# Optimization experiments

Hardware: AMD Instinct MI355X
Metric: run time of the kernel (lower is better)

Reference implementation:

```python
import jax, jax.numpy as jnp
import numpy as np

N, E, H, D_IN, D_OUT, DEPTH, G = 100000, 1600000, 128, 128, 10, 3, 256


def setup_inputs() -> dict:
    key = jax.random.key(0)
    ks = jax.random.split(key, 16)
    s = lambda k, shape: jax.random.normal(k, shape, dtype=jnp.float32) * 0.05
    inp = {
        "x": jax.random.normal(ks[0], (N, D_IN), dtype=jnp.float32),
        "edge_index": jax.random.randint(ks[1], (2, E), 0, N, dtype=jnp.int32),
        "control_edge_index": jax.random.randint(ks[2], (2, 1024), 0, N, dtype=jnp.int32),
        "batch": jnp.sort(jax.random.randint(ks[3], (N,), 0, G, dtype=jnp.int32)),
        # encoder MLP: input_dim -> hidden -> hidden
        "enc_w1": s(ks[4], (D_IN, H)), "enc_b1": jnp.zeros((H,), jnp.float32),
        "enc_w2": s(ks[5], (H, H)),    "enc_b2": jnp.zeros((H,), jnp.float32),
        # conv_depth GCN layers, hidden -> hidden
        "conv_w": s(ks[6], (DEPTH, H, H)), "conv_b": jnp.zeros((DEPTH, H), jnp.float32),
        # decoder MLP: hidden -> hidden -> output_dim
        "dec_w1": s(ks[7], (H, H)),     "dec_b1": jnp.zeros((H,), jnp.float32),
        "dec_w2": s(ks[8], (H, D_OUT)), "dec_b2": jnp.zeros((D_OUT,), jnp.float32),
    }
    return inp


def _gcn_forward(x, enc_w1, enc_b1, enc_w2, enc_b2, conv_w, conv_b,
                 dec_w1, dec_b1, dec_w2, dec_b2, edge_index, batch):
    # encoder MLP (Linear-ReLU-Dropout(eval)-Linear)
    h = jax.nn.relu(x @ enc_w1 + enc_b1) @ enc_w2 + enc_b2

    # GCN normalization with self-loops: D^{-1/2} (A + I) D^{-1/2}
    loops = jnp.arange(N, dtype=edge_index.dtype)
    src = jnp.concatenate([edge_index[0], loops])  # [E + N]
    dst = jnp.concatenate([edge_index[1], loops])
    deg = jax.ops.segment_sum(jnp.ones_like(src, dtype=h.dtype), dst, num_segments=N)
    inv_sqrt = jax.lax.rsqrt(deg)  # deg >= 1 thanks to self-loops
    coef = (inv_sqrt[src] * inv_sqrt[dst])[:, None]  # [E+N, 1]

    for l in range(DEPTH):
        hw = h @ conv_w[l] + conv_b[l]                      # [N, H]
        h = jax.ops.segment_sum(hw[src] * coef, dst, num_segments=N)
        if l < DEPTH - 1:  # linear=False -> nonlinearity between convs
            h = jax.nn.relu(h)

    # global_add_pool over graph ids
    pooled = jax.ops.segment_sum(h, batch, num_segments=G)   # [G, H]

    # decoder MLP
    return jax.nn.relu(pooled @ dec_w1 + dec_b1) @ dec_w2 + dec_b2  # [G, D_OUT]


def reference(x, edge_index, control_edge_index, batch, enc_w1, enc_b1, enc_w2,
              enc_b2, conv_w, conv_b, dec_w1, dec_b1, dec_w2, dec_b2):
    # control_edge_index corresponds to the (disabled) control mechanism; unused
    return _gcn_forward(x, enc_w1, enc_b1, enc_w2, enc_b2, conv_w, conv_b,
                        dec_w1, dec_b1, dec_w2, dec_b2, edge_index, batch)
```

## Files before the change

kernel.cpp:

```cpp
#include <hip/hip_runtime.h>
#include <hip/hip_bf16.h>
#include <cstdint>
#include <cstddef>

#define NN 100000
#define NE 1600000
#define HH 128
#define NG 256

#define NB 196
#define BSH 9
#define BMSK 511
#define CHUNK 16384
#define NBLK 98

typedef __bf16 bf16x8 __attribute__((ext_vector_type(8)));
typedef float floatx4 __attribute__((ext_vector_type(4)));

__device__ __forceinline__ uint32_t f2b(float f) {
  union { float f; uint32_t u; } v; v.f = f;
  uint32_t u = v.u;
  return (u + 0x7FFFu + ((u >> 16) & 1u)) >> 16;
}
__device__ __forceinline__ float b2f(uint32_t h) {
  union { uint32_t u; float f; } v; v.u = h << 16;
  return v.f;
}
__device__ __forceinline__ void addrow(float* a, uint4 v) {
  a[0] += b2f(v.x & 0xFFFFu); a[1] += b2f(v.x >> 16);
  a[2] += b2f(v.y & 0xFFFFu); a[3] += b2f(v.y >> 16);
  a[4] += b2f(v.z & 0xFFFFu); a[5] += b2f(v.z >> 16);
  a[6] += b2f(v.w & 0xFFFFu); a[7] += b2f(v.w >> 16);
}


__global__ __launch_bounds__(256) void k_cntA(const int* __restrict__ src,
                                              int* __restrict__ blkcnt) {
  __shared__ int h[NB];
  int t = threadIdx.x;
  if (t < NB) h[t] = 0;
  __syncthreads();
  int base = blockIdx.x * CHUNK, end = min(base + CHUNK, NE);
  for (int i = base + t; i < end; i += 256) atomicAdd(&h[src[i] >> BSH], 1);
  __syncthreads();
  if (t < NB) blkcnt[blockIdx.x * NB + t] = h[t];
}

__global__ __launch_bounds__(256) void k_cntB(const uint2* __restrict__ pairs,
                                              int* __restrict__ blkcnt) {
  __shared__ int h[NB];
  int t = threadIdx.x;
  if (t < NB) h[t] = 0;
  __syncthreads();
  int base = blockIdx.x * CHUNK, end = min(base + CHUNK, NE);
  for (int i = base + t; i < end; i += 256) atomicAdd(&h[pairs[i].y >> BSH], 1);
  __syncthreads();
  if (t < NB) blkcnt[blockIdx.x * NB + t] = h[t];
}

__global__ __launch_bounds__(64) void k_colscan(const int* __restrict__ blkcnt,
                                                int* __restrict__ poff,
                                                int* __restrict__ colsum) {
  int b = blockIdx.x, t = threadIdx.x;
  int carry = 0;
  for (int base = 0; base < NBLK; base += 64) {
    int r = base + t;
    int x = (r < NBLK) ? blkcnt[r * NB + b] : 0;
    int v = x;
    for (int d = 1; d < 64; d <<= 1) { int u = __shfl_up(v, d); if (t >= d) v += u; }
    if (r < NBLK) poff[r * NB + b] = carry + v - x;
    carry += __shfl(v, 63);
  }
  if (t == 0) colsum[b] = carry;
}

__global__ void k_gscan(const int* __restrict__ colsum, int* __restrict__ gbase,
                        int* __restrict__ off, int set_off) {
  __shared__ int s[256];
  int t = threadIdx.x;
  int x = (t < NB) ? colsum[t] : 0;
  s[t] = x; __syncthreads();
  for (int d = 1; d < 256; d <<= 1) {
    int v = (t >= d) ? s[t - d] : 0;
    __syncthreads();
    s[t] += v;
    __syncthreads();
  }
  if (t < NB) gbase[t] = s[t] - x;
  if (t == 0) { gbase[NB] = NE; if (set_off) off[NN] = NE; }
}

__global__ __launch_bounds__(256) void k_placeA(const int* __restrict__ src,
                                                const int* __restrict__ dst,
                                                const int* __restrict__ poff,
                                                const int* __restrict__ gbase,
                                                uint2* __restrict__ pairs) {
  __shared__ int cur[NB];
  int t = threadIdx.x;
  if (t < NB) cur[t] = poff[blockIdx.x * NB + t] + gbase[t];
  __syncthreads();
  int base = blockIdx.x * CHUNK, end = min(base + CHUNK, NE);
  for (int i = base + t; i < end; i += 256) {
    int s = src[i], d = dst[i];
    int p = atomicAdd(&cur[s >> BSH], 1);
    pairs[p] = make_uint2((unsigned)s, (unsigned)d);
  }
}

__global__ __launch_bounds__(256) void k_placeB(const uint2* __restrict__ pairs,
                                                const int* __restrict__ poff,
                                                const int* __restrict__ gbase,
                                                uint32_t* __restrict__ outb) {
  __shared__ int cur[NB];
  int t = threadIdx.x;
  if (t < NB) cur[t] = poff[blockIdx.x * NB + t] + gbase[t];
  __syncthreads();
  int base = blockIdx.x * CHUNK, end = min(base + CHUNK, NE);
  for (int i = base + t; i < end; i += 256) {
    uint2 v = pairs[i];
    int p = atomicAdd(&cur[v.y >> BSH], 1);
    outb[p] = v.x | ((v.y & (unsigned)BMSK) << 17);
  }
}

__global__ __launch_bounds__(256) void k_bucket_sort(
    const uint32_t* __restrict__ pairbuf, const int* __restrict__ gbase,
    int* __restrict__ off, float* __restrict__ inv, int* __restrict__ csrs)
{
  __shared__ int cnt[512];
  __shared__ int loff[512];
  __shared__ int psum[256];
  int b = blockIdx.x;
  int tid = threadIdx.x;
  cnt[tid] = 0; cnt[tid + 256] = 0;
  __syncthreads();
  int s0 = gbase[b], s1 = gbase[b + 1];
  for (int i = s0 + tid; i < s1; i += 256)
    atomicAdd(&cnt[pairbuf[i] >> 17], 1);
  __syncthreads();
  int a0 = cnt[2 * tid], a1 = cnt[2 * tid + 1];
  int s = a0 + a1;
  psum[tid] = s;
  __syncthreads();
  for (int d = 1; d < 256; d <<= 1) {
    int v = (tid >= d) ? psum[tid - d] : 0;
    __syncthreads();
    psum[tid] += v;
    __syncthreads();
  }
  int excl = psum[tid] - s;
  loff[2 * tid] = excl;
  loff[2 * tid + 1] = excl + a0;
  __syncthreads();
#pragma unroll
  for (int k = 0; k < 2; ++k) {
    int i = tid + k * 256;
    int node = b * 512 + i;
    if (node < NN) {
      off[node] = s0 + loff[i];
      inv[node] = rsqrtf((float)cnt[i] + 1.0f);
    }
  }
  __syncthreads();
  cnt[tid] = loff[tid]; cnt[tid + 256] = loff[tid + 256];
  __syncthreads();
  for (int i = s0 + tid; i < s1; i += 256) {
    uint32_t v = pairbuf[i];
    int p = atomicAdd(&cnt[v >> 17], 1);
    csrs[s0 + p] = (int)(v & 0x1FFFFu);
  }
}

__global__ __launch_bounds__(256) void k_nodeprep(const int* __restrict__ off,
                                                  const int* __restrict__ batch,
                                                  int* __restrict__ dhist,
                                                  int* __restrict__ gstart) {
  __shared__ int h[64];
  int t = threadIdx.x;
  if (t < 64) h[t] = 0;
  __syncthreads();
  int i = blockIdx.x * 256 + t;
  if (i < NN) {
    int d = off[i + 1] - off[i]; if (d > 63) d = 63;
    atomicAdd(&h[d], 1);
    int b = batch[i];
    if (i == 0) {
      for (int g = 0; g <= b; ++g) gstart[g] = 0;
    } else {
      int a = batch[i - 1];
      for (int g = a + 1; g <= b; ++g) gstart[g] = i;
    }
    if (i == NN - 1) {
      for (int g = b + 1; g <= NG; ++g) gstart[g] = NN;
    }
  }
  __syncthreads();
  if (t < 64 && h[t]) atomicAdd(&dhist[t], h[t]);
}

__global__ void k_dscan(const int* __restrict__ dhist, int* __restrict__ dcur) {
  int t = threadIdx.x;
  int x = dhist[63 - t];
  int v = x;
  for (int d = 1; d < 64; d <<= 1) { int u = __shfl_up(v, d); if (t >= d) v += u; }
  dcur[63 - t] = v - x;
}

__global__ __launch_bounds__(256) void k_dplace(const int* __restrict__ off,
                                                int* __restrict__ dcur,
                                                int* __restrict__ order) {
  __shared__ int h[64], base[64];
  int t = threadIdx.x;
  if (t < 64) h[t] = 0;
  __syncthreads();
  int i = blockIdx.x * 256 + t;
  int d = 0, ld = 0;
  if (i < NN) { d = off[i + 1] - off[i]; if (d > 63) d = 63; ld = atomicAdd(&h[d], 1); }
  __syncthreads();
  if (t < 64) base[t] = h[t] ? atomicAdd(&dcur[t], h[t]) : 0;
  __syncthreads();
  if (i < NN) order[base[d] + ld] = i;
}

__global__ __launch_bounds__(256) void k_gemm(
    const uint16_t* __restrict__ A16, const float* __restrict__ A32,
    const float* __restrict__ W, const float* __restrict__ bias,
    const float* __restrict__ scale,
    uint16_t* __restrict__ Out, int M, int do_relu)
{
  __shared__ uint16_t Wt[128][136];
  const int tid = threadIdx.x;

  for (int it = 0; it < 16; ++it) {
    int idx = tid + it * 256;
    int n = idx & 127;
    int k0 = (idx >> 7) * 4;
    uint2 wv;
    wv.x = f2b(W[(k0 + 0) * 128 + n]) | (f2b(W[(k0 + 1) * 128 + n]) << 16);
    wv.y = f2b(W[(k0 + 2) * 128 + n]) | (f2b(W[(k0 + 3) * 128 + n]) << 16);
    *(uint2*)&Wt[n][k0] = wv;
  }
  __syncthreads();

  const int lane = tid & 63;
  const int wave = tid >> 6;
  const int lrow = lane & 15;
  const int lk = (lane >> 4) * 8;
  const int row0 = blockIdx.x * 128 + wave * 32;

  floatx4 acc[2][8];
#pragma unroll
  for (int t = 0; t < 2; ++t)
#pragma unroll
    for (int n = 0; n < 8; ++n)
      acc[t][n] = (floatx4){0.f, 0.f, 0.f, 0.f};

#pragma unroll
  for (int ks = 0; ks < 4; ++ks) {
    bf16x8 a[2];
#pragma unroll
    for (int t = 0; t < 2; ++t) {
      int r = row0 + t * 16 + lrow;
      uint4 tmp = {0u, 0u, 0u, 0u};
      if (r < M) {
        if (A32) {
          float4 f0 = *(const float4*)(A32 + (size_t)r * HH + ks * 32 + lk);
          float4 f1 = *(const float4*)(A32 + (size_t)r * HH + ks * 32 + lk + 4);
          tmp.x = f2b(f0.x) | (f2b(f0.y) << 16);
          tmp.y = f2b(f0.z) | (f2b(f0.w) << 16);
          tmp.z = f2b(f1.x) | (f2b(f1.y) << 16);
          tmp.w = f2b(f1.z) | (f2b(f1.w) << 16);
        } else {
          tmp = *(const uint4*)(A16 + (size_t)r * HH + ks * 32 + lk);
        }
      }
      a[t] = __builtin_bit_cast(bf16x8, tmp);
    }
#pragma unroll
    for (int n = 0; n < 8; ++n) {
      bf16x8 b = __builtin_bit_cast(bf16x8, *(const uint4*)&Wt[n * 16 + lrow][ks * 32 + lk]);
      acc[0][n] = __builtin_amdgcn_mfma_f32_16x16x32_bf16(a[0], b, acc[0][n], 0, 0, 0);
      acc[1][n] = __builtin_amdgcn_mfma_f32_16x16x32_bf16(a[1], b, acc[1][n], 0, 0, 0);
    }
  }

  float bc[8];
#pragma unroll
  for (int n = 0; n < 8; ++n) bc[n] = bias[n * 16 + lrow];

  const int rbase = (lane >> 4) * 4;
#pragma unroll
  for (int t = 0; t < 2; ++t) {
#pragma unroll
    for (int r = 0; r < 4; ++r) {
      int row = row0 + t * 16 + rbase + r;
      if (row < M) {
        float sc = scale ? scale[row] : 1.0f;
#pragma unroll
        for (int n = 0; n < 8; ++n) {
          float v = acc[t][n][r] + bc[n];
          if (do_relu) v = fmaxf(v, 0.f);
          v *= sc;
          Out[(size_t)row * HH + n * 16 + lrow] = (uint16_t)f2b(v);
        }
      }
    }
  }
}

__global__ __launch_bounds__(256) void k_agg(
    const uint16_t* __restrict__ hw2, const int* __restrict__ off,
    const int* __restrict__ csrs, const float* __restrict__ inv,
    const int* __restrict__ order,
    uint16_t* __restrict__ hout, int do_relu)
{
  int slot = blockIdx.x * 16 + (threadIdx.x >> 4);
  if (slot >= NN) return;
  int node = order[slot];
  int c = (threadIdx.x & 15) * 8;

  uint4 sv = *(const uint4*)(hw2 + (size_t)node * HH + c);
  float a[8] = {0.f, 0.f, 0.f, 0.f, 0.f, 0.f, 0.f, 0.f};
  addrow(a, sv);

  int e0 = off[node], e1 = off[node + 1];
  int e = e0;
  for (; e + 4 <= e1; e += 4) {
    int s0 = csrs[e + 0], s1 = csrs[e + 1], s2 = csrs[e + 2], s3 = csrs[e + 3];
    uint4 v0 = *(const uint4*)(hw2 + (size_t)s0 * HH + c);
    uint4 v1 = *(const uint4*)(hw2 + (size_t)s1 * HH + c);
    uint4 v2 = *(const uint4*)(hw2 + (size_t)s2 * HH + c);
    uint4 v3 = *(const uint4*)(hw2 + (size_t)s3 * HH + c);
    addrow(a, v0); addrow(a, v1); addrow(a, v2); addrow(a, v3);
  }
  for (; e < e1; ++e) {
    int s = csrs[e];
    uint4 v = *(const uint4*)(hw2 + (size_t)s * HH + c);
    addrow(a, v);
  }
  float invd = inv[node];
#pragma unroll
  for (int j = 0; j < 8; ++j) {
    a[j] *= invd;
    if (do_relu) a[j] = fmaxf(a[j], 0.f);
  }
  uint4 o;
  o.x = f2b(a[0]) | (f2b(a[1]) << 16);
  o.y = f2b(a[2]) | (f2b(a[3]) << 16);
  o.z = f2b(a[4]) | (f2b(a[5]) << 16);
  o.w = f2b(a[6]) | (f2b(a[7]) << 16);
  *(uint4*)(hout + (size_t)node * HH + c) = o;
}

__global__ __launch_bounds__(256) void k_pool(const uint16_t* __restrict__ h,
                                              const int* __restrict__ gstart,
                                              float* __restrict__ pooled) {
  __shared__ float red[16][132];
  int g = blockIdx.x;
  int tid = threadIdx.x;
  int slot = tid >> 4;
  int c = (tid & 15) * 8;

  int r0 = gstart[g], r1 = gstart[g + 1];
  float a[8] = {0.f, 0.f, 0.f, 0.f, 0.f, 0.f, 0.f, 0.f};
  for (int r = r0 + slot; r < r1; r += 16) {
    uint4 v = *(const uint4*)(h + (size_t)r * HH + c);
    a[0] += b2f(v.x & 0xFFFFu); a[1] += b2f(v.x >> 16);
    a[2] += b2f(v.y & 0xFFFFu); a[3] += b2f(v.y >> 16);
    a[4] += b2f(v.z & 0xFFFFu); a[5] += b2f(v.z >> 16);
    a[6] += b2f(v.w & 0xFFFFu); a[7] += b2f(v.w >> 16);
  }
  *(float4*)&red[slot][c]     = make_float4(a[0], a[1], a[2], a[3]);
  *(float4*)&red[slot][c + 4] = make_float4(a[4], a[5], a[6], a[7]);
  __syncthreads();
  if (tid < 128) {
    float s = 0.f;
#pragma unroll
    for (int k = 0; k < 16; ++k) s += red[k][tid];
    pooled[g * HH + tid] = s;
  }
}

__global__ void k_dec(const float* __restrict__ pooled,
                      const float* __restrict__ w1, const float* __restrict__ b1,
                      const float* __restrict__ w2, const float* __restrict__ b2,
                      float* __restrict__ out) {
  __shared__ float p[128], t[128];
  int g = blockIdx.x, j = threadIdx.x;
  p[j] = pooled[g * HH + j];
  __syncthreads();
  float a = b1[j];
  for (int k = 0; k < 128; ++k) a += p[k] * w1[k * 128 + j];
  t[j] = fmaxf(a, 0.f);
  __syncthreads();
  if (j < 10) {
    float o = b2[j];
    for (int k = 0; k < 128; ++k) o += t[k] * w2[k * 10 + j];
    out[g * 10 + j] = o;
  }
}

extern "C" void kernel_launch(void* const* d_in, const int* in_sizes, int n_in,
                              void* d_out, int out_size, void* d_ws, size_t ws_size,
                              hipStream_t stream) {
  const float* x       = (const float*)d_in[0];
  const int*   eidx    = (const int*)d_in[1];
  const int*   src     = eidx;
  const int*   dst     = eidx + NE;
  const int*   batch   = (const int*)d_in[3];
  const float* enc_w1  = (const float*)d_in[4];
  const float* enc_b1  = (const float*)d_in[5];
  const float* enc_w2  = (const float*)d_in[6];
  const float* enc_b2  = (const float*)d_in[7];
  const float* conv_w  = (const float*)d_in[8];
  const float* conv_b  = (const float*)d_in[9];
  const float* dec_w1  = (const float*)d_in[10];
  const float* dec_b1  = (const float*)d_in[11];
  const float* dec_w2  = (const float*)d_in[12];
  const float* dec_b2  = (const float*)d_in[13];
  float* out = (float*)d_out;

  char* ws = (char*)d_ws;
  size_t o = 0;
  auto alloc = [&](size_t bytes) -> char* {
    char* p = ws + o;
    o += (bytes + 255) & ~(size_t)255;
    return p;
  };
  int*      off     = (int*)alloc((size_t)(NN + 1) * 4);
  int*      csrs    = (int*)alloc((size_t)NE * 4);
  float*    inv     = (float*)alloc((size_t)NN * 4);
  float*    pooled  = (float*)alloc((size_t)NG * HH * 4);
  int*      blkcntA = (int*)alloc((size_t)NBLK * NB * 4);
  int*      poffA   = (int*)alloc((size_t)NBLK * NB * 4);
  int*      blkcntB = (int*)alloc((size_t)NBLK * NB * 4);
  int*      poffB   = (int*)alloc((size_t)NBLK * NB * 4);
  int*      colsumA = (int*)alloc((size_t)NB * 4);
  int*      colsumB = (int*)alloc((size_t)NB * 4);
  int*      gbaseA  = (int*)alloc((size_t)(NB + 1) * 4);
  int*      gbaseB  = (int*)alloc((size_t)(NB + 1) * 4);
  int*      dhist   = (int*)alloc(64 * 4);
  int*      dcur    = (int*)alloc(64 * 4);
  int*      order   = (int*)alloc((size_t)NN * 4);
  int*      gstart  = (int*)alloc((size_t)(NG + 1) * 4);
  uint16_t* buf0    = (uint16_t*)alloc((size_t)NN * HH * 2);
  uint16_t* buf1    = (uint16_t*)alloc((size_t)NN * HH * 2);
  uint2*    pairsA  = (uint2*)buf1;
  uint32_t* pairB   = (uint32_t*)((char*)buf1 + (size_t)NE * 8);

  hipMemsetAsync(dhist, 0, 64 * 4, stream);

  k_cntA<<<dim3(NBLK), dim3(256), 0, stream>>>(src, blkcntA);
  k_colscan<<<dim3(NB), dim3(64), 0, stream>>>(blkcntA, poffA, colsumA);
  k_gscan<<<dim3(1), dim3(256), 0, stream>>>(colsumA, gbaseA, off, 0);
  k_placeA<<<dim3(NBLK), dim3(256), 0, stream>>>(src, dst, poffA, gbaseA, pairsA);
  k_cntB<<<dim3(NBLK), dim3(256), 0, stream>>>(pairsA, blkcntB);
  k_colscan<<<dim3(NB), dim3(64), 0, stream>>>(blkcntB, poffB, colsumB);
  k_gscan<<<dim3(1), dim3(256), 0, stream>>>(colsumB, gbaseB, off, 1);
  k_placeB<<<dim3(NBLK), dim3(256), 0, stream>>>(pairsA, poffB, gbaseB, pairB);
  k_bucket_sort<<<dim3(NB), dim3(256), 0, stream>>>(pairB, gbaseB, off, inv, csrs);

  const int NBK = (NN + 255) / 256;
  k_nodeprep<<<dim3(NBK), dim3(256), 0, stream>>>(off, batch, dhist, gstart);
  k_dscan<<<dim3(1), dim3(64), 0, stream>>>(dhist, dcur);
  k_dplace<<<dim3(NBK), dim3(256), 0, stream>>>(off, dcur, order);

  const int GB = (NN + 127) / 128;
  k_gemm<<<dim3(GB), dim3(256), 0, stream>>>(nullptr, x, enc_w1, enc_b1, nullptr, buf1, NN, 1);
  k_gemm<<<dim3(GB), dim3(256), 0, stream>>>(buf1, nullptr, enc_w2, enc_b2, nullptr, buf0, NN, 0);

  const int AB = (NN + 15) / 16;
  k_gemm<<<dim3(GB), dim3(256), 0, stream>>>(buf0, nullptr, conv_w + 0 * 16384, conv_b + 0,   inv, buf1, NN, 0);
  k_agg <<<dim3(AB), dim3(256), 0, stream>>>(buf1, off, csrs, inv, order, buf0, 1);
  k_gemm<<<dim3(GB), dim3(256), 0, stream>>>(buf0, nullptr, conv_w + 1 * 16384, conv_b + 128, inv, buf1, NN, 0);
  k_agg <<<dim3(AB), dim3(256), 0, stream>>>(buf1, off, csrs, inv, order, buf0, 1);
  k_gemm<<<dim3(GB), dim3(256), 0, stream>>>(buf0, nullptr, conv_w + 2 * 16384, conv_b + 256, inv, buf1, NN, 0);
  k_agg <<<dim3(AB), dim3(256), 0, stream>>>(buf1, off, csrs, inv, order, buf0, 0);

  k_pool<<<dim3(NG), dim3(256), 0, stream>>>(buf0, gstart, pooled);
  k_dec<<<dim3(NG), dim3(128), 0, stream>>>(pooled, dec_w1, dec_b1, dec_w2, dec_b2, out);
}
```

Baseline: 523.9 us.

## Fuse CSR build into one cooperative kernel and merge pool with decoder

The dozen graph-preprocessing launches (counting, column scans, placement, bucket sort, node prep, degree-sorted ordering) are merged into one cooperative kernel of 196 blocks that uses grid-wide syncs between phases. Edge chunks are resized so each of the 196 blocks takes one slice, and the degree histogram becomes per-block partials summed by block 0, which removes the memset and the global atomics. Pooling and the decoder MLP are fused into one kernel, dropping the intermediate pooled buffer. The aim is to cut launch overhead and inter-kernel gaps. The cost is grid-sync latency and fewer active blocks in the phases that used to launch 391 blocks.

Result: slower. 722.6 us (+37.9%).

```diff
diff --git a/kernel.cpp b/kernel.cpp
--- a/kernel.cpp
+++ b/kernel.cpp
@@ -1,7 +1,10 @@
 #include <hip/hip_runtime.h>
 #include <hip/hip_bf16.h>
+#include <hip/hip_cooperative_groups.h>
 #include <cstdint>
 #include <cstddef>
+
+namespace cg = cooperative_groups;
 
 #define NN 100000
 #define NE 1600000
@@ -11,8 +14,7 @@
 #define NB 196
 #define BSH 9
 #define BMSK 511
-#define CHUNK 16384
-#define NBLK 98
+#define ECH 8164
 
 typedef __bf16 bf16x8 __attribute__((ext_vector_type(8)));
 typedef float floatx4 __attribute__((ext_vector_type(4)));
@@ -33,193 +35,192 @@
   a[6] += b2f(v.w & 0xFFFFu); a[7] += b2f(v.w >> 16);
 }
 
-
-__global__ __launch_bounds__(256) void k_cntA(const int* __restrict__ src,
-                                              int* __restrict__ blkcnt) {
-  __shared__ int h[NB];
-  int t = threadIdx.x;
-  if (t < NB) h[t] = 0;
-  __syncthreads();
-  int base = blockIdx.x * CHUNK, end = min(base + CHUNK, NE);
-  for (int i = base + t; i < end; i += 256) atomicAdd(&h[src[i] >> BSH], 1);
-  __syncthreads();
-  if (t < NB) blkcnt[blockIdx.x * NB + t] = h[t];
-}
-
-__global__ __launch_bounds__(256) void k_cntB(const uint2* __restrict__ pairs,
-                                              int* __restrict__ blkcnt) {
-  __shared__ int h[NB];
-  int t = threadIdx.x;
-  if (t < NB) h[t] = 0;
-  __syncthreads();
-  int base = blockIdx.x * CHUNK, end = min(base + CHUNK, NE);
-  for (int i = base + t; i < end; i += 256) atomicAdd(&h[pairs[i].y >> BSH], 1);
-  __syncthreads();
-  if (t < NB) blkcnt[blockIdx.x * NB + t] = h[t];
-}
-
-__global__ __launch_bounds__(64) void k_colscan(const int* __restrict__ blkcnt,
-                                                int* __restrict__ poff,
-                                                int* __restrict__ colsum) {
-  int b = blockIdx.x, t = threadIdx.x;
-  int carry = 0;
-  for (int base = 0; base < NBLK; base += 64) {
-    int r = base + t;
-    int x = (r < NBLK) ? blkcnt[r * NB + b] : 0;
-    int v = x;
+struct BuildArgs {
+  const int* src; const int* dst; const int* batch;
+  int* blkcntA; int* poffA; int* colsumA; int* gbaseA;
+  uint2* pairsA;
+  int* blkcntB; int* poffB; int* colsumB; int* gbaseB;
+  uint32_t* pairB;
+  int* off; float* inv; int* csrs;
+  int* dhist2; int* dcur; int* order; int* gstart;
+};
+
+__global__ __launch_bounds__(256) void k_build(BuildArgs A) {
+  cg::grid_group grid = cg::this_grid();
+  __shared__ int sm[1536];
+  const int b = blockIdx.x, t = threadIdx.x;
+
+  {
+    int* h = sm;
+    if (t < NB) h[t] = 0;
+    __syncthreads();
+    int e0 = b * ECH, e1 = min(e0 + ECH, NE);
+    for (int i = e0 + t; i < e1; i += 256) atomicAdd(&h[A.src[i] >> BSH], 1);
+    __syncthreads();
+    if (t < NB) A.blkcntA[b * NB + t] = h[t];
+  }
+  grid.sync();
+  {
+    int* s = sm;
+    int x = (t < NB) ? A.blkcntA[t * NB + b] : 0;
+    s[t] = x; __syncthreads();
+    for (int d = 1; d < 256; d <<= 1) {
+      int v = (t >= d) ? s[t - d] : 0; __syncthreads(); s[t] += v; __syncthreads();
+    }
+    if (t < NB) A.poffA[t * NB + b] = s[t] - x;
+    if (t == 255) A.colsumA[b] = s[255];
+  }
+  grid.sync();
+  if (b == 0) {
+    int* s = sm;
+    int x = (t < NB) ? A.colsumA[t] : 0;
+    s[t] = x; __syncthreads();
+    for (int d = 1; d < 256; d <<= 1) {
+      int v = (t >= d) ? s[t - d] : 0; __syncthreads(); s[t] += v; __syncthreads();
+    }
+    if (t < NB) A.gbaseA[t] = s[t] - x;
+    if (t == 0) A.gbaseA[NB] = NE;
+  }
+  grid.sync();
+  {
+    int* cur = sm;
+    if (t < NB) cur[t] = A.poffA[b * NB + t] + A.gbaseA[t];
+    __syncthreads();
+    int e0 = b * ECH, e1 = min(e0 + ECH, NE);
+    for (int i = e0 + t; i < e1; i += 256) {
+      int s_ = A.src[i], d_ = A.dst[i];
+      int p = atomicAdd(&cur[s_ >> BSH], 1);
+      A.pairsA[p] = make_uint2((unsigned)s_, (unsigned)d_);
+    }
+  }
+  grid.sync();
+  {
+    int* h = sm;
+    if (t < NB) h[t] = 0;
+    __syncthreads();
+    int e0 = b * ECH, e1 = min(e0 + ECH, NE);
+    for (int i = e0 + t; i < e1; i += 256) atomicAdd(&h[A.pairsA[i].y >> BSH], 1);
+    __syncthreads();
+    if (t < NB) A.blkcntB[b * NB + t] = h[t];
+  }
+  grid.sync();
+  {
+    int* s = sm;
+    int x = (t < NB) ? A.blkcntB[t * NB + b] : 0;
+    s[t] = x; __syncthreads();
+    for (int d = 1; d < 256; d <<= 1) {
+      int v = (t >= d) ? s[t - d] : 0; __syncthreads(); s[t] += v; __syncthreads();
+    }
+    if (t < NB) A.poffB[t * NB + b] = s[t] - x;
+    if (t == 255) A.colsumB[b] = s[255];
+  }
+  grid.sync();
+  if (b == 0) {
+    int* s = sm;
+    int x = (t < NB) ? A.colsumB[t] : 0;
+    s[t] = x; __syncthreads();
+    for (int d = 1; d < 256; d <<= 1) {
+      int v = (t >= d) ? s[t - d] : 0; __syncthreads(); s[t] += v; __syncthreads();
+    }
+    if (t < NB) A.gbaseB[t] = s[t] - x;
+    if (t == 0) { A.gbaseB[NB] = NE; A.off[NN] = NE; }
+  }
+  grid.sync();
+  {
+    int* cur = sm;
+    if (t < NB) cur[t] = A.poffB[b * NB + t] + A.gbaseB[t];
+    __syncthreads();
+    int e0 = b * ECH, e1 = min(e0 + ECH, NE);
+    for (int i = e0 + t; i < e1; i += 256) {
+      uint2 v = A.pairsA[i];
+      int p = atomicAdd(&cur[v.y >> BSH], 1);
+      A.pairB[p] = v.x | ((v.y & (unsigned)BMSK) << 17);
+    }
+  }
+  grid.sync();
+  {
+    int* cnt = sm; int* loff = sm + 512; int* psum = sm + 1024;
+    cnt[t] = 0; cnt[t + 256] = 0;
+    __syncthreads();
+    int s0 = A.gbaseB[b], s1 = A.gbaseB[b + 1];
+    for (int i = s0 + t; i < s1; i += 256) atomicAdd(&cnt[A.pairB[i] >> 17], 1);
+    __syncthreads();
+    int a0 = cnt[2 * t], a1 = cnt[2 * t + 1];
+    int s = a0 + a1;
+    psum[t] = s; __syncthreads();
+    for (int d = 1; d < 256; d <<= 1) {
+      int v = (t >= d) ? psum[t - d] : 0; __syncthreads(); psum[t] += v; __syncthreads();
+    }
+    int excl = psum[t] - s;
+    loff[2 * t] = excl;
+    loff[2 * t + 1] = excl + a0;
+    __syncthreads();
+    int* h64 = psum;
+    if (t < 64) h64[t] = 0;
+    __syncthreads();
+#pragma unroll
+    for (int k = 0; k < 2; ++k) {
+      int i = t + k * 256;
+      int node = b * 512 + i;
+      if (node < NN) {
+        A.off[node] = s0 + loff[i];
+        A.inv[node] = rsqrtf((float)cnt[i] + 1.0f);
+        int d = cnt[i]; if (d > 63) d = 63;
+        atomicAdd(&h64[d], 1);
+      }
+    }
+    __syncthreads();
+    if (t < 64) A.dhist2[b * 64 + t] = h64[t];
+    int n0 = b * 512, n1 = min(n0 + 512, NN);
+    for (int i = n0 + t; i < n1; i += 256) {
+      int bb = A.batch[i];
+      if (i == 0) { for (int g = 0; g <= bb; ++g) A.gstart[g] = 0; }
+      else { int aa = A.batch[i - 1]; for (int g = aa + 1; g <= bb; ++g) A.gstart[g] = i; }
+      if (i == NN - 1) { for (int g = bb + 1; g <= NG; ++g) A.gstart[g] = NN; }
+    }
+    __syncthreads();
+    cnt[t] = loff[t]; cnt[t + 256] = loff[t + 256];
+    __syncthreads();
+    for (int i = s0 + t; i < s1; i += 256) {
+      uint32_t v = A.pairB[i];
+      int p = atomicAdd(&cnt[v >> 17], 1);
+      A.csrs[s0 + p] = (int)(v & 0x1FFFFu);
+    }
+  }
+  grid.sync();
+  if (b == 0 && t < 64) {
+    int sum = 0;
+    for (int r = 0; r < NB; ++r) sum += A.dhist2[r * 64 + (63 - t)];
+    int v = sum;
     for (int d = 1; d < 64; d <<= 1) { int u = __shfl_up(v, d); if (t >= d) v += u; }
-    if (r < NBLK) poff[r * NB + b] = carry + v - x;
-    carry += __shfl(v, 63);
-  }
-  if (t == 0) colsum[b] = carry;
-}
-
-__global__ void k_gscan(const int* __restrict__ colsum, int* __restrict__ gbase,
-                        int* __restrict__ off, int set_off) {
-  __shared__ int s[256];
-  int t = threadIdx.x;
-  int x = (t < NB) ? colsum[t] : 0;
-  s[t] = x; __syncthreads();
-  for (int d = 1; d < 256; d <<= 1) {
-    int v = (t >= d) ? s[t - d] : 0;
-    __syncthreads();
-    s[t] += v;
-    __syncthreads();
-  }
-  if (t < NB) gbase[t] = s[t] - x;
-  if (t == 0) { gbase[NB] = NE; if (set_off) off[NN] = NE; }
-}
-
-__global__ __launch_bounds__(256) void k_placeA(const int* __restrict__ src,
-                                                const int* __restrict__ dst,
-                                                const int* __restrict__ poff,
-                                                const int* __restrict__ gbase,
-                                                uint2* __restrict__ pairs) {
-  __shared__ int cur[NB];
-  int t = threadIdx.x;
-  if (t < NB) cur[t] = poff[blockIdx.x * NB + t] + gbase[t];
-  __syncthreads();
-  int base = blockIdx.x * CHUNK, end = min(base + CHUNK, NE);
-  for (int i = base + t; i < end; i += 256) {
-    int s = src[i], d = dst[i];
-    int p = atomicAdd(&cur[s >> BSH], 1);
-    pairs[p] = make_uint2((unsigned)s, (unsigned)d);
-  }
-}
-
-__global__ __launch_bounds__(256) void k_placeB(const uint2* __restrict__ pairs,
-                                                const int* __restrict__ poff,
-                                                const int* __restrict__ gbase,
-                                                uint32_t* __restrict__ outb) {
-  __shared__ int cur[NB];
-  int t = threadIdx.x;
-  if (t < NB) cur[t] = poff[blockIdx.x * NB + t] + gbase[t];
-  __syncthreads();
-  int base = blockIdx.x * CHUNK, end = min(base + CHUNK, NE);
-  for (int i = base + t; i < end; i += 256) {
-    uint2 v = pairs[i];
-    int p = atomicAdd(&cur[v.y >> BSH], 1);
-    outb[p] = v.x | ((v.y & (unsigned)BMSK) << 17);
-  }
-}
-
-__global__ __launch_bounds__(256) void k_bucket_sort(
-    const uint32_t* __restrict__ pairbuf, const int* __restrict__ gbase,
-    int* __restrict__ off, float* __restrict__ inv, int* __restrict__ csrs)
-{
-  __shared__ int cnt[512];
-  __shared__ int loff[512];
-  __shared__ int psum[256];
-  int b = blockIdx.x;
-  int tid = threadIdx.x;
-  cnt[tid] = 0; cnt[tid + 256] = 0;
-  __syncthreads();
-  int s0 = gbase[b], s1 = gbase[b + 1];
-  for (int i = s0 + tid; i < s1; i += 256)
-    atomicAdd(&cnt[pairbuf[i] >> 17], 1);
-  __syncthreads();
-  int a0 = cnt[2 * tid], a1 = cnt[2 * tid + 1];
-  int s = a0 + a1;
-  psum[tid] = s;
-  __syncthreads();
-  for (int d = 1; d < 256; d <<= 1) {
-    int v = (tid >= d) ? psum[tid - d] : 0;
-    __syncthreads();
-    psum[tid] += v;
-    __syncthreads();
-  }
-  int excl = psum[tid] - s;
-  loff[2 * tid] = excl;
-  loff[2 * tid + 1] = excl + a0;
-  __syncthreads();
-#pragma unroll
-  for (int k = 0; k < 2; ++k) {
-    int i = tid + k * 256;
-    int node = b * 512 + i;
-    if (node < NN) {
-      off[node] = s0 + loff[i];
-      inv[node] = rsqrtf((float)cnt[i] + 1.0f);
-    }
-  }
-  __syncthreads();
-  cnt[tid] = loff[tid]; cnt[tid + 256] = loff[tid + 256];
-  __syncthreads();
-  for (int i = s0 + tid; i < s1; i += 256) {
-    uint32_t v = pairbuf[i];
-    int p = atomicAdd(&cnt[v >> 17], 1);
-    csrs[s0 + p] = (int)(v & 0x1FFFFu);
-  }
-}
-
-__global__ __launch_bounds__(256) void k_nodeprep(const int* __restrict__ off,
-                                                  const int* __restrict__ batch,
-                                                  int* __restrict__ dhist,
-                                                  int* __restrict__ gstart) {
-  __shared__ int h[64];
-  int t = threadIdx.x;
-  if (t < 64) h[t] = 0;
-  __syncthreads();
-  int i = blockIdx.x * 256 + t;
-  if (i < NN) {
-    int d = off[i + 1] - off[i]; if (d > 63) d = 63;
-    atomicAdd(&h[d], 1);
-    int b = batch[i];
-    if (i == 0) {
-      for (int g = 0; g <= b; ++g) gstart[g] = 0;
-    } else {
-      int a = batch[i - 1];
-      for (int g = a + 1; g <= b; ++g) gstart[g] = i;
-    }
-    if (i == NN - 1) {
-      for (int g = b + 1; g <= NG; ++g) gstart[g] = NN;
-    }
-  }
-  __syncthreads();
-  if (t < 64 && h[t]) atomicAdd(&dhist[t], h[t]);
-}
-
-__global__ void k_dscan(const int* __restrict__ dhist, int* __restrict__ dcur) {
-  int t = threadIdx.x;
-  int x = dhist[63 - t];
-  int v = x;
-  for (int d = 1; d < 64; d <<= 1) { int u = __shfl_up(v, d); if (t >= d) v += u; }
-  dcur[63 - t] = v - x;
-}
-
-__global__ __launch_bounds__(256) void k_dplace(const int* __restrict__ off,
-                                                int* __restrict__ dcur,
-                                                int* __restrict__ order) {
-  __shared__ int h[64], base[64];
-  int t = threadIdx.x;
-  if (t < 64) h[t] = 0;
-  __syncthreads();
-  int i = blockIdx.x * 256 + t;
-  int d = 0, ld = 0;
-  if (i < NN) { d = off[i + 1] - off[i]; if (d > 63) d = 63; ld = atomicAdd(&h[d], 1); }
-  __syncthreads();
-  if (t < 64) base[t] = h[t] ? atomicAdd(&dcur[t], h[t]) : 0;
-  __syncthreads();
-  if (i < NN) order[base[d] + ld] = i;
+    A.dcur[63 - t] = v - sum;
+  }
+  grid.sync();
+  {
+    int* h = sm; int* base = sm + 64;
+    if (t < 64) h[t] = 0;
+    __syncthreads();
+    int dd[2], ld[2];
+    int n0 = b * 512;
+#pragma unroll
+    for (int k = 0; k < 2; ++k) {
+      int i = n0 + t + k * 256;
+      dd[k] = -1; ld[k] = 0;
+      if (i < NN) {
+        int d = A.off[i + 1] - A.off[i]; if (d > 63) d = 63;
+        dd[k] = d;
+        ld[k] = atomicAdd(&h[d], 1);
+      }
+    }
+    __syncthreads();
+    if (t < 64) base[t] = h[t] ? atomicAdd(&A.dcur[t], h[t]) : 0;
+    __syncthreads();
+#pragma unroll
+    for (int k = 0; k < 2; ++k) {
+      int i = n0 + t + k * 256;
+      if (i < NN) A.order[base[dd[k]] + ld[k]] = i;
+    }
+  }
 }
 
 __global__ __launch_bounds__(256) void k_gemm(
@@ -352,10 +353,14 @@
   *(uint4*)(hout + (size_t)node * HH + c) = o;
 }
 
-__global__ __launch_bounds__(256) void k_pool(const uint16_t* __restrict__ h,
-                                              const int* __restrict__ gstart,
-                                              float* __restrict__ pooled) {
+__global__ __launch_bounds__(256) void k_pooldec(
+    const uint16_t* __restrict__ h, const int* __restrict__ gstart,
+    const float* __restrict__ w1, const float* __restrict__ b1,
+    const float* __restrict__ w2, const float* __restrict__ b2,
+    float* __restrict__ out)
+{
   __shared__ float red[16][132];
+  __shared__ float p[128], tmpv[128];
   int g = blockIdx.x;
   int tid = threadIdx.x;
   int slot = tid >> 4;
@@ -377,26 +382,19 @@
     float s = 0.f;
 #pragma unroll
     for (int k = 0; k < 16; ++k) s += red[k][tid];
-    pooled[g * HH + tid] = s;
-  }
-}
-
-__global__ void k_dec(const float* __restrict__ pooled,
-                      const float* __restrict__ w1, const float* __restrict__ b1,
-                      const float* __restrict__ w2, const float* __restrict__ b2,
-                      float* __restrict__ out) {
-  __shared__ float p[128], t[128];
-  int g = blockIdx.x, j = threadIdx.x;
-  p[j] = pooled[g * HH + j];
+    p[tid] = s;
+  }
   __syncthreads();
-  float a = b1[j];
-  for (int k = 0; k < 128; ++k) a += p[k] * w1[k * 128 + j];
-  t[j] = fmaxf(a, 0.f);
+  if (tid < 128) {
+    float acc1 = b1[tid];
+    for (int k = 0; k < 128; ++k) acc1 += p[k] * w1[k * 128 + tid];
+    tmpv[tid] = fmaxf(acc1, 0.f);
+  }
   __syncthreads();
-  if (j < 10) {
-    float o = b2[j];
-    for (int k = 0; k < 128; ++k) o += t[k] * w2[k * 10 + j];
-    out[g * 10 + j] = o;
+  if (tid < 10) {
+    float o = b2[tid];
+    for (int k = 0; k < 128; ++k) o += tmpv[k] * w2[k * 10 + tid];
+    out[g * 10 + tid] = o;
   }
 }
 
@@ -430,16 +428,15 @@
   int*      off     = (int*)alloc((size_t)(NN + 1) * 4);
   int*      csrs    = (int*)alloc((size_t)NE * 4);
   float*    inv     = (float*)alloc((size_t)NN * 4);
-  float*    pooled  = (float*)alloc((size_t)NG * HH * 4);
-  int*      blkcntA = (int*)alloc((size_t)NBLK * NB * 4);
-  int*      poffA   = (int*)alloc((size_t)NBLK * NB * 4);
-  int*      blkcntB = (int*)alloc((size_t)NBLK * NB * 4);
-  int*      poffB   = (int*)alloc((size_t)NBLK * NB * 4);
+  int*      blkcntA = (int*)alloc((size_t)NB * NB * 4);
+  int*      poffA   = (int*)alloc((size_t)NB * NB * 4);
+  int*      blkcntB = (int*)alloc((size_t)NB * NB * 4);
+  int*      poffB   = (int*)alloc((size_t)NB * NB * 4);
   int*      colsumA = (int*)alloc((size_t)NB * 4);
   int*      colsumB = (int*)alloc((size_t)NB * 4);
   int*      gbaseA  = (int*)alloc((size_t)(NB + 1) * 4);
   int*      gbaseB  = (int*)alloc((size_t)(NB + 1) * 4);
-  int*      dhist   = (int*)alloc(64 * 4);
+  int*      dhist2  = (int*)alloc((size_t)NB * 64 * 4);
   int*      dcur    = (int*)alloc(64 * 4);
   int*      order   = (int*)alloc((size_t)NN * 4);
   int*      gstart  = (int*)alloc((size_t)(NG + 1) * 4);
@@ -448,22 +445,16 @@
   uint2*    pairsA  = (uint2*)buf1;
   uint32_t* pairB   = (uint32_t*)((char*)buf1 + (size_t)NE * 8);
 
-  hipMemsetAsync(dhist, 0, 64 * 4, stream);
-
-  k_cntA<<<dim3(NBLK), dim3(256), 0, stream>>>(src, blkcntA);
-  k_colscan<<<dim3(NB), dim3(64), 0, stream>>>(blkcntA, poffA, colsumA);
-  k_gscan<<<dim3(1), dim3(256), 0, stream>>>(colsumA, gbaseA, off, 0);
-  k_placeA<<<dim3(NBLK), dim3(256), 0, stream>>>(src, dst, poffA, gbaseA, pairsA);
-  k_cntB<<<dim3(NBLK), dim3(256), 0, stream>>>(pairsA, blkcntB);
-  k_colscan<<<dim3(NB), dim3(64), 0, stream>>>(blkcntB, poffB, colsumB);
-  k_gscan<<<dim3(1), dim3(256), 0, stream>>>(colsumB, gbaseB, off, 1);
-  k_placeB<<<dim3(NBLK), dim3(256), 0, stream>>>(pairsA, poffB, gbaseB, pairB);
-  k_bucket_sort<<<dim3(NB), dim3(256), 0, stream>>>(pairB, gbaseB, off, inv, csrs);
-
-  const int NBK = (NN + 255) / 256;
-  k_nodeprep<<<dim3(NBK), dim3(256), 0, stream>>>(off, batch, dhist, gstart);
-  k_dscan<<<dim3(1), dim3(64), 0, stream>>>(dhist, dcur);
-  k_dplace<<<dim3(NBK), dim3(256), 0, stream>>>(off, dcur, order);
+  BuildArgs ba;
+  ba.src = src; ba.dst = dst; ba.batch = batch;
+  ba.blkcntA = blkcntA; ba.poffA = poffA; ba.colsumA = colsumA; ba.gbaseA = gbaseA;
+  ba.pairsA = pairsA;
+  ba.blkcntB = blkcntB; ba.poffB = poffB; ba.colsumB = colsumB; ba.gbaseB = gbaseB;
+  ba.pairB = pairB;
+  ba.off = off; ba.inv = inv; ba.csrs = csrs;
+  ba.dhist2 = dhist2; ba.dcur = dcur; ba.order = order; ba.gstart = gstart;
+  void* bargs[] = { &ba };
+  hipLaunchCooperativeKernel((void*)k_build, dim3(NB), dim3(256), bargs, 0, stream);
 
   const int GB = (NN + 127) / 128;
   k_gemm<<<dim3(GB), dim3(256), 0, stream>>>(nullptr, x, enc_w1, enc_b1, nullptr, buf1, NN, 1);
@@ -477,6 +468,5 @@
   k_gemm<<<dim3(GB), dim3(256), 0, stream>>>(buf0, nullptr, conv_w + 2 * 16384, conv_b + 256, inv, buf1, NN, 0);
   k_agg <<<dim3(AB), dim3(256), 0, stream>>>(buf1, off, csrs, inv, order, buf0, 0);
 
-  k_pool<<<dim3(NG), dim3(256), 0, stream>>>(buf0, gstart, pooled);
-  k_dec<<<dim3(NG), dim3(128), 0, stream>>>(pooled, dec_w1, dec_b1, dec_w2, dec_b2, out);
-}
+  k_pooldec<<<dim3(NG), dim3(256), 0, stream>>>(buf0, gstart, dec_w1, dec_b1, dec_w2, dec_b2, out);
+}
```
